# Optimization experiments

Hardware: AMD Instinct MI355X
Metric: run time of the kernel (lower is better)

## Reference

```python
import jax, jax.numpy as jnp
import numpy as np

N, E, D_IN, D_OUT, H = 50000, 800000, 128, 128, 4
D_H = D_OUT // H


def setup_inputs() -> dict:
    key = jax.random.key(0)
    ks = jax.random.split(key, 6)
    x = jax.random.normal(ks[0], (N, D_IN), dtype=jnp.float32)
    edge_index = jax.random.randint(ks[1], (2, E), 0, N, dtype=jnp.int64)
    # parameters (xavier-ish scaling)
    W = jax.random.normal(ks[2], (D_IN, D_OUT), dtype=jnp.float32) * (1.0 / np.sqrt(D_IN))
    attn_vec = jax.random.normal(ks[3], (H, 2 * D_H), dtype=jnp.float32) * (1.0 / np.sqrt(2 * D_H))
    out_w = jax.random.normal(ks[4], (D_OUT, D_OUT), dtype=jnp.float32) * (1.0 / np.sqrt(D_OUT))
    out_b = jax.random.normal(ks[5], (D_OUT,), dtype=jnp.float32) * 0.01
    return {"x": x, "edge_index": edge_index, "W": W, "attn_vec": attn_vec,
            "out_w": out_w, "out_b": out_b}


def reference(x, edge_index, W, attn_vec, out_w, out_b):
    n = x.shape[0]
    Wx = (x @ W).reshape(n, H, D_H)                      # [N,H,d_h]
    src, dst = edge_index[0], edge_index[1]
    h_src = Wx[src]                                      # [E,H,d_h]
    h_dst = Wx[dst]                                      # [E,H,d_h]
    a_i = attn_vec[:, :D_H]                              # [H,d_h]
    a_j = attn_vec[:, D_H:]                              # [H,d_h]
    e = jnp.einsum('ehd,hd->eh', h_src, a_i) + jnp.einsum('ehd,hd->eh', h_dst, a_j)
    e = jax.nn.leaky_relu(e, negative_slope=0.2)         # [E,H]
    # segment softmax over incoming edges per destination node
    e_max = jax.ops.segment_max(e, dst, num_segments=n)  # [N,H]
    exp_e = jnp.exp(e - e_max[dst])                      # [E,H]
    exp_sum = jax.ops.segment_sum(exp_e, dst, num_segments=n)  # [N,H]
    alpha = exp_e / (exp_sum[dst] + 1e-16)               # [E,H]
    # weighted scatter-add aggregation
    agg = jax.ops.segment_sum(alpha[:, :, None] * h_src, dst, num_segments=n)  # [N,H,d_h]
    out = agg.reshape(n, D_OUT) @ out_w + out_b
    return jax.nn.elu(out)
```

## Files before the change

kernel.cpp:

```cpp
#include <hip/hip_runtime.h>
#include <math.h>


typedef __attribute__((ext_vector_type(8))) short short8;
typedef __attribute__((ext_vector_type(4))) float f32x4;

#define BIN_VPT 16

__device__ __forceinline__ float lrelu(float v) { return v >= 0.f ? v : 0.2f * v; }

__device__ __forceinline__ unsigned short f2bf(float f) {
  unsigned int u = __float_as_uint(f);
  u += 0x7FFFu + ((u >> 16) & 1u);
  return (unsigned short)(u >> 16);
}
__device__ __forceinline__ unsigned int cvt_pk_bf16(float lo, float hi) {
  unsigned int r;
  asm("v_cvt_pk_bf16_f32 %0, %1, %2" : "=v"(r) : "v"(lo), "v"(hi));
  return r;
}
__device__ __forceinline__ float bflo(unsigned int w) { return __uint_as_float(w << 16); }
__device__ __forceinline__ float bfhi(unsigned int w) { return __uint_as_float(w & 0xFFFF0000u); }

__device__ __forceinline__ int blk_excl_scan(int v, int* ws) {
  const int t = threadIdx.x, lane = t & 63, wv = t >> 6;
  int incl = v;
#pragma unroll
  for (int m = 1; m < 64; m <<= 1) {
    int x = __shfl_up(incl, m, 64);
    if (lane >= m) incl += x;
  }
  if (lane == 63) ws[wv] = incl;
  __syncthreads();
  int woff = 0;
  for (int p = 0; p < wv; ++p) woff += ws[p];
  return woff + incl - v;
}

__global__ void k_setup(const float* __restrict__ W, const float* __restrict__ ow,
                        const float* __restrict__ attn,
                        unsigned short* __restrict__ wf, unsigned short* __restrict__ owf,
                        unsigned short* __restrict__ abf,
                        int* __restrict__ gcnt, int* __restrict__ gcur) {
  __shared__ float Mw[128][16];
  if (blockIdx.x == 16) {
    const int t = threadIdx.x;
    if (t < 128) {
      float v[16];
#pragma unroll
      for (int c = 0; c < 16; ++c) v[c] = 0.f;
#pragma unroll
      for (int h = 0; h < 4; ++h) {
        float si = 0.f, sj = 0.f;
        for (int dd = 0; dd < 32; ++dd) {
          const float w = W[t * 128 + h * 32 + dd];
          si += w * attn[h * 64 + dd];
          sj += w * attn[h * 64 + 32 + dd];
        }
        v[h] = si;
        v[4 + h] = sj;
      }
#pragma unroll
      for (int c = 0; c < 16; ++c) Mw[t][c] = v[c];
    }
    __syncthreads();
    const int lane = t & 63;
    const int ks = t >> 6;
    const int k0 = ks * 32 + (lane >> 4) * 8;
    const int col = lane & 15;
    short8 vv;
#pragma unroll
    for (int j = 0; j < 8; ++j) vv[j] = (short)f2bf(Mw[k0 + j][col]);
    *(short8*)(abf + ((size_t)(ks * 64 + lane)) * 8) = vv;
    return;
  }
  const int t = blockIdx.x * 256 + threadIdx.x;
  if (blockIdx.x == 0) gcnt[threadIdx.x] = 0;
  if (blockIdx.x == 1) gcur[threadIdx.x] = 0;
  const int which = t >> 11;
  const int tt = t & 2047;
  const float* M = which ? ow : W;
  unsigned short* F = which ? owf : wf;
  const int lane = tt & 63;
  const int nt = (tt >> 6) & 7;
  const int ks = tt >> 9;
  const int k0 = ks * 32 + (lane >> 4) * 8;
  const int col = nt * 16 + (lane & 15);
  short8 v;
#pragma unroll
  for (int j = 0; j < 8; ++j) v[j] = (short)f2bf(M[(k0 + j) * 128 + col]);
  *(short8*)(F + (size_t)tt * 8) = v;
}

__global__ void k_gemm1b(const float* __restrict__ x, const unsigned short* __restrict__ wf,
                         const unsigned short* __restrict__ abf,
                         unsigned int* __restrict__ Wxb,
                         float* __restrict__ s_i, float* __restrict__ s_j, int n,
                         const int* __restrict__ dst, int* __restrict__ gcnt, int E,
                         int gemmBlocks) {
  __shared__ int lc[256];
  if (blockIdx.x >= gemmBlocks) {
    const int bb = blockIdx.x - gemmBlocks;
    lc[threadIdx.x] = 0;
    __syncthreads();
    const int base = bb * (256 * BIN_VPT);
#pragma unroll
    for (int j = 0; j < BIN_VPT; ++j) {
      int e = base + j * 256 + threadIdx.x;
      if (e < E) atomicAdd(&lc[((unsigned int)dst[e]) >> 8], 1);
    }
    __syncthreads();
    int c = lc[threadIdx.x];
    if (c) atomicAdd(&gcnt[threadIdx.x], c);
    return;
  }

  const int lane = threadIdx.x & 63;
  const int gw = blockIdx.x * (blockDim.x >> 6) + (threadIdx.x >> 6);
  const int r0 = gw * 16;
  if (r0 >= n) return;
  const int g = lane >> 4, c = lane & 15;

  f32x4 acc[8];
#pragma unroll
  for (int nt = 0; nt < 8; ++nt) acc[nt] = (f32x4){0.f, 0.f, 0.f, 0.f};
  f32x4 sacc = (f32x4){0.f, 0.f, 0.f, 0.f};

  const int arow = min(r0 + c, n - 1);
#pragma unroll
  for (int ks = 0; ks < 4; ++ks) {
    const float* xr = x + (size_t)arow * 128 + ks * 32 + g * 8;
    float4 v0 = *(const float4*)xr;
    float4 v1 = *(const float4*)(xr + 4);
    uint4 au;
    au.x = cvt_pk_bf16(v0.x, v0.y);
    au.y = cvt_pk_bf16(v0.z, v0.w);
    au.z = cvt_pk_bf16(v1.x, v1.y);
    au.w = cvt_pk_bf16(v1.z, v1.w);
    short8 af = __builtin_bit_cast(short8, au);
#pragma unroll
    for (int nt = 0; nt < 8; ++nt) {
      short8 bf = *(const short8*)(wf + ((size_t)(ks * 8 + nt) * 64 + lane) * 8);
      acc[nt] = __builtin_amdgcn_mfma_f32_16x16x32_bf16(af, bf, acc[nt], 0, 0, 0);
    }
    short8 ab = *(const short8*)(abf + ((size_t)(ks * 64 + lane)) * 8);
    sacc = __builtin_amdgcn_mfma_f32_16x16x32_bf16(af, ab, sacc, 0, 0, 0);
  }

  const int odd = c & 1;
#pragma unroll
  for (int r = 0; r < 4; ++r) {
    const int row = r0 + g * 4 + r;
    if (row >= n) continue;
    unsigned int* dp = Wxb + (size_t)row * 64;
#pragma unroll
    for (int ntp = 0; ntp < 4; ++ntp) {
      float ve = acc[ntp][r], vo = acc[ntp + 4][r];
      float vex = __shfl_xor(ve, 1, 64);
      float vox = __shfl_xor(vo, 1, 64);
      const int nt = odd ? ntp + 4 : ntp;
      dp[nt * 8 + (c >> 1)] = cvt_pk_bf16(odd ? vox : ve, odd ? vo : vex);
    }
  }

#pragma unroll
  for (int r = 0; r < 4; ++r) {
    const int row = r0 + g * 4 + r;
    if (row < n) {
      if (c < 4)      s_i[(size_t)row * 4 + c] = sacc[r];
      else if (c < 8) s_j[(size_t)row * 4 + (c - 4)] = sacc[r];
    }
  }
}

__global__ void k_bin1(const int* __restrict__ edges, const int* __restrict__ gcnt,
                       int* __restrict__ gcur, unsigned int* __restrict__ tmp, int E) {
  __shared__ int ws[4];
  __shared__ int bst_s[256];
  __shared__ int lcnt[256];
  __shared__ int lbase[256];
  const int t = threadIdx.x;
  const int excl = blk_excl_scan(gcnt[t], ws);
  bst_s[t] = excl;
  lcnt[t] = 0;
  __syncthreads();
  const int base = blockIdx.x * (256 * BIN_VPT);
  unsigned int pv[BIN_VPT];
  int rk[BIN_VPT];
#pragma unroll
  for (int j = 0; j < BIN_VPT; ++j) {
    int e = base + j * 256 + t;
    if (e < E) {
      unsigned int s = (unsigned int)edges[e];
      unsigned int d = (unsigned int)edges[E + e];
      pv[j] = s | (d << 16);
      rk[j] = atomicAdd(&lcnt[d >> 8], 1);
    } else {
      pv[j] = 0u;
      rk[j] = -1;
    }
  }
  __syncthreads();
  const int c = lcnt[t];
  lbase[t] = bst_s[t] + (c ? atomicAdd(&gcur[t], c) : 0);
  __syncthreads();
#pragma unroll
  for (int j = 0; j < BIN_VPT; ++j) {
    if (rk[j] >= 0) {
      const int b = pv[j] >> 24;
      tmp[lbase[b] + rk[j]] = pv[j];
    }
  }
}

__global__ void k_bin2(const unsigned int* __restrict__ tmp, const int* __restrict__ gcnt,
                       int* __restrict__ csr, int* __restrict__ offs,
                       int* __restrict__ cnts, int n) {
  __shared__ int ws[4];
  __shared__ int bst_s[256];
  __shared__ int nc[256];
  const int b = blockIdx.x;
  const int t = threadIdx.x;
  bst_s[t] = blk_excl_scan(gcnt[t], ws);
  nc[t] = 0;
  __syncthreads();
  const int base = bst_s[b], cnt = gcnt[b];
  for (int i = t; i < cnt; i += 256)
    atomicAdd(&nc[(tmp[base + i] >> 16) & 255], 1);
  __syncthreads();
  const int node = b * 256 + t;
  const int c = nc[t];
  if (node < n) cnts[node] = c;
  __syncthreads();
  const int excl = blk_excl_scan(c, ws);
  if (node < n) offs[node] = base + excl;
  __syncthreads();
  nc[t] = excl;
  __syncthreads();
  for (int i = t; i < cnt; i += 256) {
    unsigned int v = tmp[base + i];
    int pos = atomicAdd(&nc[(v >> 16) & 255], 1);
    csr[base + pos] = (int)(v & 0xFFFFu);
  }
}

#define AGG_EDGE(e)                                                     \
  {                                                                     \
    int s_ = lsrc[wv][e];                                               \
    float p_ = lp[wv][e][h];                                            \
    unsigned int w_ = Wxb[(unsigned)(s_ << 6) | (unsigned)lane];        \
    acc.x += p_ * bflo(w_);                                             \
    acc.y += p_ * bfhi(w_);                                             \
    smh += p_;                                                          \
  }

__global__ void k_aggm(const unsigned int* __restrict__ Wxb, const float* __restrict__ s_i,
                       const float* __restrict__ s_j, const int* __restrict__ offs,
                       const int* __restrict__ cnts, const int* __restrict__ csr_src,
                       const unsigned short* __restrict__ owf, const float* __restrict__ ob,
                       float* __restrict__ out, int n) {
  __shared__ unsigned int aTile[16][65];
  __shared__ int   lsrc[4][64];
  __shared__ float lp[4][64][4];
  const int lane = threadIdx.x & 63;
  const int wv = threadIdx.x >> 6;
  const int nd0 = blockIdx.x * 16;
  const int nd0w = nd0 + wv * 4;
  const int h = lane >> 4;

  int degv = 0;
  if (lane < 4 && nd0w + lane < n) degv = cnts[nd0w + lane];
  const int wbase = (nd0w < n) ? offs[nd0w] : 0;
  const int d0 = __shfl(degv, 0, 64), d1 = __shfl(degv, 1, 64);
  const int d2 = __shfl(degv, 2, 64), d3 = __shfl(degv, 3, 64);
  const int b0 = d0, b1 = d0 + d1, b2 = b1 + d2;
  const int tot = b2 + d3;

  int cur = 0;
  int rem = d0;
  float2 acc = make_float2(0.f, 0.f);
  float smh = 0.f;

  while (cur < 4 && rem == 0) {
    if (nd0w + cur < n) aTile[(wv << 2) + cur][lane] = 0u;
    ++cur;
    rem = (cur == 1) ? d1 : (cur == 2) ? d2 : (cur == 3) ? d3 : 0;
  }

  for (int c0 = 0; c0 < tot; c0 += 64) {
    const int m = min(64, tot - c0);
    if (lane < m) {
      const int pos = c0 + lane;
      const int src = csr_src[wbase + pos];
      const int nl = (pos >= b0) + (pos >= b1) + (pos >= b2);
      const float4 sj = *(const float4*)(s_j + (size_t)(nd0w + nl) * 4);
      const float4 si = *(const float4*)(s_i + (size_t)src * 4);
      float4 p;
      p.x = __expf(lrelu(si.x + sj.x));
      p.y = __expf(lrelu(si.y + sj.y));
      p.z = __expf(lrelu(si.z + sj.z));
      p.w = __expf(lrelu(si.w + sj.w));
      lsrc[wv][lane] = src;
      *(float4*)&lp[wv][lane][0] = p;
    }
    asm volatile("s_waitcnt lgkmcnt(0)" ::: "memory");
    int k = 0;
    while (k < m) {
      const int take = min(m - k, rem);
      int e = k;
      const int end = k + take;
      for (; e + 8 <= end; e += 8) {
        AGG_EDGE(e + 0) AGG_EDGE(e + 1) AGG_EDGE(e + 2) AGG_EDGE(e + 3)
        AGG_EDGE(e + 4) AGG_EDGE(e + 5) AGG_EDGE(e + 6) AGG_EDGE(e + 7)
      }
      for (; e + 4 <= end; e += 4) {
        AGG_EDGE(e + 0) AGG_EDGE(e + 1) AGG_EDGE(e + 2) AGG_EDGE(e + 3)
      }
      for (; e < end; ++e) AGG_EDGE(e)
      k += take;
      rem -= take;
      while (rem == 0 && cur < 4) {
        const float inv = 1.f / (smh + 1e-16f);
        if (nd0w + cur < n)
          aTile[(wv << 2) + cur][lane] = cvt_pk_bf16(acc.x * inv, acc.y * inv);
        ++cur;
        acc.x = 0.f; acc.y = 0.f; smh = 0.f;
        rem = (cur == 1) ? d1 : (cur == 2) ? d2 : (cur == 3) ? d3 : 0;
      }
      if (cur >= 4) break;
    }
  }
  __syncthreads();

  const int g = lane >> 4, c = lane & 15;
#pragma unroll
  for (int t2 = 0; t2 < 2; ++t2) {
    const int nt = wv + t2 * 4;
    f32x4 o = (f32x4){0.f, 0.f, 0.f, 0.f};
#pragma unroll
    for (int ks = 0; ks < 4; ++ks) {
      uint4 au = *(const uint4*)&aTile[c][ks * 16 + g * 4];
      short8 af = __builtin_bit_cast(short8, au);
      short8 bf = *(const short8*)(owf + ((size_t)(ks * 8 + nt) * 64 + lane) * 8);
      o = __builtin_amdgcn_mfma_f32_16x16x32_bf16(af, bf, o, 0, 0, 0);
    }
#pragma unroll
    for (int r = 0; r < 4; ++r) {
      const int row = nd0 + g * 4 + r;
      if (row < n) {
        float v = o[r] + ob[nt * 16 + c];
        v = v > 0.f ? v : expm1f(v);
        out[(size_t)row * 128 + nt * 16 + c] = v;
      }
    }
  }
}

extern "C" void kernel_launch(void* const* d_in, const int* in_sizes, int n_in,
                              void* d_out, int out_size, void* d_ws, size_t ws_size,
                              hipStream_t stream) {
  const float* x    = (const float*)d_in[0];
  const int*   edges = (const int*)d_in[1];
  const float* W    = (const float*)d_in[2];
  const float* attn = (const float*)d_in[3];
  const float* ow   = (const float*)d_in[4];
  const float* ob   = (const float*)d_in[5];
  const int n = in_sizes[0] / 128;
  const int E = in_sizes[1] / 2;
  float* out = (float*)d_out;

  char* wp = (char*)d_ws;
  auto alloc = [&](size_t bytes) {
    char* p = wp;
    wp += (bytes + 255) & ~(size_t)255;
    return p;
  };
  unsigned short* wf  = (unsigned short*)alloc(2048 * 8 * 2);
  unsigned short* owf = (unsigned short*)alloc(2048 * 8 * 2);
  unsigned short* abf = (unsigned short*)alloc(256 * 8 * 2);
  unsigned int*   Wxb = (unsigned int*)alloc((size_t)n * 64 * 4);
  float* s_i    = (float*)alloc((size_t)n * 4 * 4);
  float* s_j    = (float*)alloc((size_t)n * 4 * 4);
  int*   gcnt   = (int*)alloc(256 * 4);
  int*   gcur   = (int*)alloc(256 * 4);
  int*   offs   = (int*)alloc((size_t)n * 4);
  int*   cnts   = (int*)alloc((size_t)n * 4);
  unsigned int* tmp = (unsigned int*)alloc((size_t)E * 4);
  int*   csr    = (int*)alloc((size_t)E * 4);

  dim3 blk(256);
  const int NB = (n + 255) / 256;
  const int EB = (E + 256 * BIN_VPT - 1) / (256 * BIN_VPT);
  const int strips = (n + 15) / 16;
  const int gemmBlocks = (strips + 3) / 4;

  k_setup<<<17, blk, 0, stream>>>(W, ow, attn, wf, owf, abf, gcnt, gcur);
  k_gemm1b<<<gemmBlocks + EB, blk, 0, stream>>>(x, wf, abf, Wxb, s_i, s_j, n,
                                                edges + E, gcnt, E, gemmBlocks);
  k_bin1<<<EB, blk, 0, stream>>>(edges, gcnt, gcur, tmp, E);
  k_bin2<<<NB, blk, 0, stream>>>(tmp, gcnt, csr, offs, cnts, n);
  k_aggm<<<(n + 15) / 16, blk, 0, stream>>>(Wxb, s_i, s_j, offs, cnts, csr,
                                            owf, ob, out, n);
}
```

Baseline: 93.30 us.

## Move edge histogram into setup kernel and fuse binning pass with GEMM

Measured after the change: 91.70 us. Within noise of the previous version (-1.7%).

```diff
diff --git a/kernel.cpp b/kernel.cpp
--- a/kernel.cpp
+++ b/kernel.cpp
@@ -37,12 +37,28 @@
   return woff + incl - v;
 }
 
-__global__ void k_setup(const float* __restrict__ W, const float* __restrict__ ow,
-                        const float* __restrict__ attn,
-                        unsigned short* __restrict__ wf, unsigned short* __restrict__ owf,
-                        unsigned short* __restrict__ abf,
-                        int* __restrict__ gcnt, int* __restrict__ gcur) {
+__global__ void k_su_hist(const float* __restrict__ W, const float* __restrict__ ow,
+                          const float* __restrict__ attn,
+                          unsigned short* __restrict__ wf, unsigned short* __restrict__ owf,
+                          unsigned short* __restrict__ abf,
+                          const int* __restrict__ dst, int* __restrict__ gcnt, int E) {
   __shared__ float Mw[128][16];
+  __shared__ int lc[256];
+  if (blockIdx.x >= 17) {
+    const int bb = blockIdx.x - 17;
+    lc[threadIdx.x] = 0;
+    __syncthreads();
+    const int base = bb * (256 * BIN_VPT);
+#pragma unroll
+    for (int j = 0; j < BIN_VPT; ++j) {
+      int e = base + j * 256 + threadIdx.x;
+      if (e < E) atomicAdd(&lc[((unsigned int)dst[e]) >> 8], 1);
+    }
+    __syncthreads();
+    int c = lc[threadIdx.x];
+    if (c) atomicAdd(&gcnt[threadIdx.x], c);
+    return;
+  }
   if (blockIdx.x == 16) {
     const int t = threadIdx.x;
     if (t < 128) {
@@ -64,8 +80,9 @@
       for (int c = 0; c < 16; ++c) Mw[t][c] = v[c];
     }
     __syncthreads();
-    const int lane = t & 63;
-    const int ks = t >> 6;
+    const int t2 = threadIdx.x;
+    const int lane = t2 & 63;
+    const int ks = t2 >> 6;
     const int k0 = ks * 32 + (lane >> 4) * 8;
     const int col = lane & 15;
     short8 vv;
@@ -75,8 +92,6 @@
     return;
   }
   const int t = blockIdx.x * 256 + threadIdx.x;
-  if (blockIdx.x == 0) gcnt[threadIdx.x] = 0;
-  if (blockIdx.x == 1) gcur[threadIdx.x] = 0;
   const int which = t >> 11;
   const int tt = t & 2047;
   const float* M = which ? ow : W;
@@ -92,26 +107,51 @@
   *(short8*)(F + (size_t)tt * 8) = v;
 }
 
-__global__ void k_gemm1b(const float* __restrict__ x, const unsigned short* __restrict__ wf,
-                         const unsigned short* __restrict__ abf,
-                         unsigned int* __restrict__ Wxb,
-                         float* __restrict__ s_i, float* __restrict__ s_j, int n,
-                         const int* __restrict__ dst, int* __restrict__ gcnt, int E,
-                         int gemmBlocks) {
-  __shared__ int lc[256];
+__global__ void k_g1_bin1(const float* __restrict__ x, const unsigned short* __restrict__ wf,
+                          const unsigned short* __restrict__ abf,
+                          unsigned int* __restrict__ Wxb,
+                          float* __restrict__ s_i, float* __restrict__ s_j, int n,
+                          const int* __restrict__ edges, const int* __restrict__ gcnt,
+                          int* __restrict__ gcur, unsigned int* __restrict__ tmp, int E,
+                          int gemmBlocks) {
+  __shared__ int ws[4];
+  __shared__ int bst_s[256];
+  __shared__ int lcnt[256];
+  __shared__ int lbase[256];
   if (blockIdx.x >= gemmBlocks) {
     const int bb = blockIdx.x - gemmBlocks;
-    lc[threadIdx.x] = 0;
+    const int t = threadIdx.x;
+    const int excl = blk_excl_scan(gcnt[t], ws);
+    bst_s[t] = excl;
+    lcnt[t] = 0;
     __syncthreads();
     const int base = bb * (256 * BIN_VPT);
+    unsigned int pv[BIN_VPT];
+    int rk[BIN_VPT];
 #pragma unroll
     for (int j = 0; j < BIN_VPT; ++j) {
-      int e = base + j * 256 + threadIdx.x;
-      if (e < E) atomicAdd(&lc[((unsigned int)dst[e]) >> 8], 1);
-    }
-    __syncthreads();
-    int c = lc[threadIdx.x];
-    if (c) atomicAdd(&gcnt[threadIdx.x], c);
+      int e = base + j * 256 + t;
+      if (e < E) {
+        unsigned int s = (unsigned int)edges[e];
+        unsigned int d = (unsigned int)edges[E + e];
+        pv[j] = s | (d << 16);
+        rk[j] = atomicAdd(&lcnt[d >> 8], 1);
+      } else {
+        pv[j] = 0u;
+        rk[j] = -1;
+      }
+    }
+    __syncthreads();
+    const int c = lcnt[t];
+    lbase[t] = bst_s[t] + (c ? atomicAdd(&gcur[t], c) : 0);
+    __syncthreads();
+#pragma unroll
+    for (int j = 0; j < BIN_VPT; ++j) {
+      if (rk[j] >= 0) {
+        const int b = pv[j] >> 24;
+        tmp[lbase[b] + rk[j]] = pv[j];
+      }
+    }
     return;
   }
 
@@ -169,46 +209,6 @@
     if (row < n) {
       if (c < 4)      s_i[(size_t)row * 4 + c] = sacc[r];
       else if (c < 8) s_j[(size_t)row * 4 + (c - 4)] = sacc[r];
-    }
-  }
-}
-
-__global__ void k_bin1(const int* __restrict__ edges, const int* __restrict__ gcnt,
-                       int* __restrict__ gcur, unsigned int* __restrict__ tmp, int E) {
-  __shared__ int ws[4];
-  __shared__ int bst_s[256];
-  __shared__ int lcnt[256];
-  __shared__ int lbase[256];
-  const int t = threadIdx.x;
-  const int excl = blk_excl_scan(gcnt[t], ws);
-  bst_s[t] = excl;
-  lcnt[t] = 0;
-  __syncthreads();
-  const int base = blockIdx.x * (256 * BIN_VPT);
-  unsigned int pv[BIN_VPT];
-  int rk[BIN_VPT];
-#pragma unroll
-  for (int j = 0; j < BIN_VPT; ++j) {
-    int e = base + j * 256 + t;
-    if (e < E) {
-      unsigned int s = (unsigned int)edges[e];
-      unsigned int d = (unsigned int)edges[E + e];
-      pv[j] = s | (d << 16);
-      rk[j] = atomicAdd(&lcnt[d >> 8], 1);
-    } else {
-      pv[j] = 0u;
-      rk[j] = -1;
-    }
-  }
-  __syncthreads();
-  const int c = lcnt[t];
-  lbase[t] = bst_s[t] + (c ? atomicAdd(&gcur[t], c) : 0);
-  __syncthreads();
-#pragma unroll
-  for (int j = 0; j < BIN_VPT; ++j) {
-    if (rk[j] >= 0) {
-      const int b = pv[j] >> 24;
-      tmp[lbase[b] + rk[j]] = pv[j];
     }
   }
 }
@@ -394,10 +394,12 @@
   const int strips = (n + 15) / 16;
   const int gemmBlocks = (strips + 3) / 4;
 
-  k_setup<<<17, blk, 0, stream>>>(W, ow, attn, wf, owf, abf, gcnt, gcur);
-  k_gemm1b<<<gemmBlocks + EB, blk, 0, stream>>>(x, wf, abf, Wxb, s_i, s_j, n,
-                                                edges + E, gcnt, E, gemmBlocks);
-  k_bin1<<<EB, blk, 0, stream>>>(edges, gcnt, gcur, tmp, E);
+  hipMemsetAsync(gcnt, 0, 2048, stream);
+  k_su_hist<<<17 + EB, blk, 0, stream>>>(W, ow, attn, wf, owf, abf,
+                                         edges + E, gcnt, E);
+  k_g1_bin1<<<gemmBlocks + EB, blk, 0, stream>>>(x, wf, abf, Wxb, s_i, s_j, n,
+                                                 edges, gcnt, gcur, tmp, E,
+                                                 gemmBlocks);
   k_bin2<<<NB, blk, 0, stream>>>(tmp, gcnt, csr, offs, cnts, n);
   k_aggm<<<(n + 15) / 16, blk, 0, stream>>>(Wxb, s_i, s_j, offs, cnts, csr,
                                             owf, ob, out, n);
```
